# Performance work log

Hardware: AMD Instinct MI355X
Metric: run time of the kernel (lower is better)

Reference implementation:

```python
import jax, jax.numpy as jnp
import numpy as np

EMSIZE = 1024
NHEAD = 16
HEAD = EMSIZE // NHEAD


def setup_inputs() -> dict:
    key = jax.random.key(0)
    ks = jax.random.split(key, 8)
    s = 1.0 / np.sqrt(EMSIZE)
    return {
        "embed": jax.random.normal(ks[0], (2, 2048, EMSIZE), dtype=jnp.float32),
        "q": jax.random.normal(ks[1], (2, 2048, EMSIZE), dtype=jnp.float32),
        "Wk": jax.random.normal(ks[2], (EMSIZE, EMSIZE), dtype=jnp.float32) * s,
        "bk": jnp.zeros((EMSIZE,), dtype=jnp.float32),
        "Wq": jax.random.normal(ks[3], (EMSIZE, EMSIZE), dtype=jnp.float32) * s,
        "bq": jnp.zeros((EMSIZE,), dtype=jnp.float32),
        "Wv": jax.random.normal(ks[4], (EMSIZE, EMSIZE), dtype=jnp.float32) * s,
        "bv": jnp.zeros((EMSIZE,), dtype=jnp.float32),
    }


def _split_heads(x):
    # [b, s, E] -> [b, h, s, d]
    b, s, _ = x.shape
    return x.reshape(b, s, NHEAD, HEAD).transpose(0, 2, 1, 3)


def reference(embed, q, Wk, bk, Wq, bq, Wv, bv):
    # torch Linear: y = x @ W.T + b
    k = _split_heads(embed @ Wk.T + bk)   # [b, h, skv, d]
    qh = _split_heads(q @ Wq.T + bq)      # [b, h, sq, d]
    v = _split_heads(embed @ Wv.T + bv)   # [b, h, skv, d]
    scale = 1.0 / np.sqrt(HEAD).astype(np.float32)
    scores = jnp.einsum("bhqd,bhkd->bhqk", qh, k) * scale
    attn = jax.nn.softmax(scores, axis=-1)  # dropout p=0 -> identity
    ctx = jnp.einsum("bhqk,bhkd->bhqd", attn, v)
    b, h, sq, d = ctx.shape
    return ctx.transpose(0, 2, 1, 3).reshape(b, sq, h * d)
```

## Files before the change

### kernel.cpp

```cpp
#include <hip/hip_runtime.h>
#include <cstdint>
#include <cstddef>


using bf16 = __bf16;
typedef __bf16 bf16x8 __attribute__((ext_vector_type(8)));
typedef float f32x4 __attribute__((ext_vector_type(4)));
typedef float f32x16 __attribute__((ext_vector_type(16)));
using uint32 = unsigned int;

__device__ __forceinline__ void async16(void* lds, const void* g) {
  __builtin_amdgcn_global_load_lds((__attribute__((address_space(1))) void*)g,
                                   (__attribute__((address_space(3))) void*)lds,
                                   16, 0, 0);
}

__device__ __forceinline__ uint32 pack_bf16x2(float lo, float hi_) {
  union { bf16 h[2]; uint32 u; } w;
  w.h[0] = (bf16)lo; w.h[1] = (bf16)hi_;
  return w.u;
}

__global__ void cast_all_kernel(const float* __restrict__ e, const float* __restrict__ q,
                                const float* __restrict__ wk, const float* __restrict__ wq,
                                const float* __restrict__ wv, bf16* __restrict__ dst) {
  int i = blockIdx.x * blockDim.x + threadIdx.x;
  if (i >= 2883584) return;
  const float* src; int off;
  if (i < 1048576)      { src = e;  off = 0; }
  else if (i < 2097152) { src = q;  off = 1048576; }
  else if (i < 2359296) { src = wk; off = 2097152; }
  else if (i < 2621440) { src = wq; off = 2359296; }
  else                  { src = wv; off = 2621440; }
  float4 v = reinterpret_cast<const float4*>(src)[i - off];
  union { bf16 h[4]; unsigned long long u; } o;
  o.h[0] = (bf16)v.x; o.h[1] = (bf16)v.y; o.h[2] = (bf16)v.z; o.h[3] = (bf16)v.w;
  reinterpret_cast<unsigned long long*>(dst)[i] = o.u;
}

__global__ __launch_bounds__(256) void proj_kernel(
    const bf16* __restrict__ emb, const bf16* __restrict__ qin,
    const bf16* __restrict__ wk, const bf16* __restrict__ wq, const bf16* __restrict__ wv,
    const float* __restrict__ bk, const float* __restrict__ bq, const float* __restrict__ bv,
    bf16* __restrict__ Kp, bf16* __restrict__ Qp, bf16* __restrict__ Vt)
{
  __shared__ bf16 As[128 * 64];
  __shared__ bf16 Bs[128 * 64];

  int pid = blockIdx.x;
  int proj = pid >> 8;
  int t = pid & 255;
  int m0 = (t >> 3) * 128;
  int n0 = (t & 7) * 128;

  const bf16* A = (proj == 1) ? qin : emb;
  const bf16* W = (proj == 0) ? wk : (proj == 1) ? wq : wv;
  const float* bias = (proj == 0) ? bk : (proj == 1) ? bq : bv;
  const bool proj2 = (proj == 2);

  int tid = threadIdx.x;
  int lane = tid & 63, wid = tid >> 6;
  int quad = lane >> 4, l16 = lane & 15;
  int moff = (wid & 1) * 64, noff = (wid >> 1) * 64;

  f32x4 zero = {0.f, 0.f, 0.f, 0.f};
  f32x4 acc[4][4];
#pragma unroll
  for (int i = 0; i < 4; i++)
#pragma unroll
    for (int j = 0; j < 4; j++) acc[i][j] = zero;

  for (int kk = 0; kk < 1024; kk += 64) {
    __syncthreads();
#pragma unroll
    for (int i = 0; i < 4; i++) {
      int c = i * 256 + tid;
      int row = c >> 3;
      int ko = ((c ^ row) & 7) << 3;
      async16(&As[(size_t)(i * 256 + wid * 64) * 8], &A[(size_t)(m0 + row) * 1024 + kk + ko]);
      async16(&Bs[(size_t)(i * 256 + wid * 64) * 8], &W[(size_t)(n0 + row) * 1024 + kk + ko]);
    }
    __syncthreads();
#pragma unroll
    for (int ks = 0; ks < 2; ks++) {
      bf16x8 af[4], bfr[4];
#pragma unroll
      for (int i = 0; i < 4; i++) {
        int row = moff + i * 16 + l16;
        af[i] = *reinterpret_cast<const bf16x8*>(&As[row * 64 + ((((ks << 2) | quad) ^ row) & 7) * 8]);
      }
#pragma unroll
      for (int j = 0; j < 4; j++) {
        int row = noff + j * 16 + l16;
        bfr[j] = *reinterpret_cast<const bf16x8*>(&Bs[row * 64 + ((((ks << 2) | quad) ^ row) & 7) * 8]);
      }
      if (proj2) {
#pragma unroll
        for (int i = 0; i < 4; i++)
#pragma unroll
          for (int j = 0; j < 4; j++)
            acc[i][j] = __builtin_amdgcn_mfma_f32_16x16x32_bf16(bfr[j], af[i], acc[i][j], 0, 0, 0);
      } else {
#pragma unroll
        for (int i = 0; i < 4; i++)
#pragma unroll
          for (int j = 0; j < 4; j++)
            acc[i][j] = __builtin_amdgcn_mfma_f32_16x16x32_bf16(af[i], bfr[j], acc[i][j], 0, 0, 0);
      }
    }
  }

  if (proj2) {
#pragma unroll
    for (int i = 0; i < 4; i++) {
      int grow = m0 + moff + i * 16 + l16;
      int bb = grow >> 11;
      int ss = grow & 2047;
#pragma unroll
      for (int j = 0; j < 4; j++) {
#pragma unroll
        for (int r = 0; r < 4; r++) {
          int gcol = n0 + noff + j * 16 + quad * 4 + r;
          int hh = gcol >> 6, dd = gcol & 63;
          int bh = bb * 16 + hh;
          float v = acc[i][j][r] + bias[gcol];
          Vt[((size_t)bh * 64 + dd) * 2048 + ss] = (bf16)v;
        }
      }
    }
  } else {
    float bvv[4];
#pragma unroll
    for (int j = 0; j < 4; j++) bvv[j] = bias[n0 + noff + j * 16 + l16];
    bf16* dst = (proj == 0) ? Kp : Qp;
    const float qs = (proj == 1) ? 0.18033688011112042f : 1.0f;
#pragma unroll
    for (int i = 0; i < 4; i++) {
#pragma unroll
      for (int r = 0; r < 4; r++) {
        int grow = m0 + moff + i * 16 + quad * 4 + r;
        int bb = grow >> 11;
        int ss = grow & 2047;
#pragma unroll
        for (int j = 0; j < 4; j++) {
          int gcol = n0 + noff + j * 16 + l16;
          int hh = gcol >> 6, dd = gcol & 63;
          int bh = bb * 16 + hh;
          float v = (acc[i][j][r] + bvv[j]) * qs;
          dst[((size_t)bh * 2048 + ss) * 64 + dd] = (bf16)v;
        }
      }
    }
  }
}

__global__ __launch_bounds__(512, 4) void attn_kernel(
    const bf16* __restrict__ Qp, const bf16* __restrict__ Kp, const bf16* __restrict__ Vt,
    float* __restrict__ out, float* __restrict__ part1, float* __restrict__ lbuf)
{
  __shared__ bf16 Ks[2][64 * 64];
  __shared__ bf16 Vs[2][64 * 64];

  int bid = blockIdx.x;
  int half = bid & 1;
  int q0 = ((bid >> 1) & 7) << 8;
  int bh = bid >> 4;
  int bb = bh >> 4, hh = bh & 15;
  int g0 = half << 4;

  const bf16* Qg = Qp + (size_t)bh * (2048 * 64);
  const bf16* Kg = Kp + (size_t)bh * (2048 * 64);
  const bf16* Vg = Vt + (size_t)bh * (64 * 2048);

  int tid = threadIdx.x, lane = tid & 63, wid = tid >> 6;
  int l32 = lane & 31;
  int h = lane >> 5;
  int wq0 = q0 + wid * 32;

  auto stage = [&](int kt_, int buf) {
    int c = tid;
    int row = c >> 3;
    int srow = (row & ~12) | ((row & 4) << 1) | ((row & 8) >> 1);
    int ko = ((c ^ row) & 7) << 3;
    async16(&Ks[buf][(size_t)(wid * 64) * 8], &Kg[(size_t)(kt_ * 64 + srow) * 64 + ko]);
    async16(&Vs[buf][(size_t)(wid * 64) * 8], &Vg[(size_t)row * 2048 + kt_ * 64 + ko]);
  };

  bf16x8 qf[4];
#pragma unroll
  for (int s = 0; s < 4; s++)
    qf[s] = *reinterpret_cast<const bf16x8*>(
        &Qg[(size_t)(wq0 + l32) * 64 + s * 16 + h * 8]);

  stage(g0, 0);

  const f32x16 z16 = {0.f, 0.f, 0.f, 0.f, 0.f, 0.f, 0.f, 0.f,
                      0.f, 0.f, 0.f, 0.f, 0.f, 0.f, 0.f, 0.f};
  f32x16 Ov[2];
  Ov[0] = z16; Ov[1] = z16;
  float2 l2;
  l2.x = 0.f; l2.y = 0.f;

  for (int kt = 0; kt < 16; kt++) {
    int cur = kt & 1;
    __syncthreads();
    __builtin_amdgcn_sched_barrier(0);
    if (kt < 15) stage(g0 + kt + 1, cur ^ 1);
    __builtin_amdgcn_sched_barrier(0);

    const bf16* Kc = Ks[cur];
    const bf16* Vc = Vs[cur];

#pragma unroll
    for (int t = 0; t < 2; t++) {
      f32x16 St;
      int row = t * 32 + l32;
      {
        bf16x8 kf = *reinterpret_cast<const bf16x8*>(&Kc[row * 64 + ((h ^ row) & 7) * 8]);
        St = __builtin_amdgcn_mfma_f32_32x32x16_bf16(kf, qf[0], z16, 0, 0, 0);
      }
#pragma unroll
      for (int s = 1; s < 4; s++) {
        int j8 = s * 2 + h;
        bf16x8 kf = *reinterpret_cast<const bf16x8*>(&Kc[row * 64 + ((j8 ^ row) & 7) * 8]);
        St = __builtin_amdgcn_mfma_f32_32x32x16_bf16(kf, qf[s], St, 0, 0, 0);
      }

      uint32 pk[8];
#pragma unroll
      for (int i = 0; i < 8; i++) {
        float pe = __builtin_amdgcn_exp2f(St[2 * i]);
        float po = __builtin_amdgcn_exp2f(St[2 * i + 1]);
        l2.x += pe; l2.y += po;
        pk[i] = pack_bf16x2(pe, po);
      }

#pragma unroll
      for (int g = 0; g < 2; g++) {
        union { uint32 u[4]; bf16x8 v; } pb;
#pragma unroll
        for (int i = 0; i < 4; i++) pb.u[i] = pk[g * 4 + i];
        int j8 = t * 4 + g * 2 + h;
#pragma unroll
        for (int dt = 0; dt < 2; dt++) {
          int rowv = dt * 32 + l32;
          bf16x8 vf = *reinterpret_cast<const bf16x8*>(&Vc[rowv * 64 + ((j8 ^ rowv) & 7) * 8]);
          Ov[dt] = __builtin_amdgcn_mfma_f32_32x32x16_bf16(vf, pb.v, Ov[dt], 0, 0, 0);
        }
      }
    }
  }

  {
    float l_half = l2.x + l2.y;
    float l_tot = l_half + __shfl_xor(l_half, 32);
    int q = wq0 + l32;
    float* dstO = (half == 0 ? out : part1) + ((size_t)bb * 2048 + q) * 1024 + hh * 64;
#pragma unroll
    for (int dt = 0; dt < 2; dt++)
#pragma unroll
      for (int g = 0; g < 4; g++) {
        float4 o;
        o.x = Ov[dt][4 * g + 0];
        o.y = Ov[dt][4 * g + 1];
        o.z = Ov[dt][4 * g + 2];
        o.w = Ov[dt][4 * g + 3];
        *reinterpret_cast<float4*>(&dstO[dt * 32 + g * 8 + 4 * h]) = o;
      }
    if (h == 0) lbuf[half * 65536 + (bh << 11) + q] = l_tot;
  }
}

__global__ __launch_bounds__(256) void combine_kernel(
    float* __restrict__ out, const float* __restrict__ part1,
    const float* __restrict__ lbuf) {
  int i = blockIdx.x * 256 + threadIdx.x;
  int e = i << 2;
  int brow = e >> 10;
  int b = brow >> 11;
  int hcol = (e >> 6) & 15;
  int srow = brow & 2047;
  int lidx = ((b * 16 + hcol) << 11) + srow;
  float inv = 1.0f / (lbuf[lidx] + lbuf[65536 + lidx]);
  float4 a = reinterpret_cast<const float4*>(out)[i];
  float4 p = reinterpret_cast<const float4*>(part1)[i];
  float4 r;
  r.x = (a.x + p.x) * inv;
  r.y = (a.y + p.y) * inv;
  r.z = (a.z + p.z) * inv;
  r.w = (a.w + p.w) * inv;
  reinterpret_cast<float4*>(out)[i] = r;
}

extern "C" void kernel_launch(void* const* d_in, const int* in_sizes, int n_in,
                              void* d_out, int out_size, void* d_ws, size_t ws_size,
                              hipStream_t stream) {
  (void)in_sizes; (void)n_in; (void)out_size; (void)ws_size;
  const float* embed = (const float*)d_in[0];
  const float* qin   = (const float*)d_in[1];
  const float* Wk    = (const float*)d_in[2];
  const float* bk    = (const float*)d_in[3];
  const float* Wq    = (const float*)d_in[4];
  const float* bq    = (const float*)d_in[5];
  const float* Wv    = (const float*)d_in[6];
  const float* bv    = (const float*)d_in[7];
  float* out = (float*)d_out;

  bf16* ws = (bf16*)d_ws;
  bf16* emb_bf = ws;
  bf16* q_bf   = emb_bf + 4194304;
  bf16* wk_bf  = q_bf   + 4194304;
  bf16* wq_bf  = wk_bf  + 1048576;
  bf16* wv_bf  = wq_bf  + 1048576;
  bf16* Kp     = wv_bf  + 1048576;
  bf16* Qp     = Kp     + 4194304;
  bf16* Vt     = Qp     + 4194304;

  float* part1 = (float*)d_ws;
  float* lbuf  = part1 + 4194304;

  cast_all_kernel<<<11264, 256, 0, stream>>>(embed, qin, Wk, Wq, Wv, ws);

  proj_kernel<<<768, 256, 0, stream>>>(emb_bf, q_bf, wk_bf, wq_bf, wv_bf,
                                       bk, bq, bv, Kp, Qp, Vt);
  attn_kernel<<<512, 512, 0, stream>>>(Qp, Kp, Vt, out, part1, lbuf);
  combine_kernel<<<4096, 256, 0, stream>>>(out, part1, lbuf);
}
```

Baseline: 192.5 us.

## Drop split-KV attention and combine kernel; each block covers full key range

Each attention block now processes 128 queries over all 32 key tiles with 256 threads, instead of splitting the key range in two across blocks. The softmax normalisation moves into the attention epilogue, so the separate combine kernel and the fp32 partial-output and row-sum buffers go away. A block-index swizzle spreads consecutive blocks across heads. This removes a launch and roughly two full fp32 output passes through memory, but each block now runs a serial loop twice as long, with fewer waves per block staging the tiles.

```diff
diff --git a/kernel.cpp b/kernel.cpp
--- a/kernel.cpp
+++ b/kernel.cpp
@@ -154,19 +154,18 @@
   }
 }
 
-__global__ __launch_bounds__(512, 4) void attn_kernel(
+__global__ __launch_bounds__(256, 2) void attn_kernel(
     const bf16* __restrict__ Qp, const bf16* __restrict__ Kp, const bf16* __restrict__ Vt,
-    float* __restrict__ out, float* __restrict__ part1, float* __restrict__ lbuf)
+    float* __restrict__ out)
 {
   __shared__ bf16 Ks[2][64 * 64];
   __shared__ bf16 Vs[2][64 * 64];
 
-  int bid = blockIdx.x;
-  int half = bid & 1;
-  int q0 = ((bid >> 1) & 7) << 8;
-  int bh = bid >> 4;
+  int swz = (blockIdx.x & 7) * 64 + (blockIdx.x >> 3);
+  int qblk = swz & 15;
+  int bh = swz >> 4;
+  int q0 = qblk << 7;
   int bb = bh >> 4, hh = bh & 15;
-  int g0 = half << 4;
 
   const bf16* Qg = Qp + (size_t)bh * (2048 * 64);
   const bf16* Kg = Kp + (size_t)bh * (2048 * 64);
@@ -178,12 +177,15 @@
   int wq0 = q0 + wid * 32;
 
   auto stage = [&](int kt_, int buf) {
-    int c = tid;
-    int row = c >> 3;
-    int srow = (row & ~12) | ((row & 4) << 1) | ((row & 8) >> 1);
-    int ko = ((c ^ row) & 7) << 3;
-    async16(&Ks[buf][(size_t)(wid * 64) * 8], &Kg[(size_t)(kt_ * 64 + srow) * 64 + ko]);
-    async16(&Vs[buf][(size_t)(wid * 64) * 8], &Vg[(size_t)row * 2048 + kt_ * 64 + ko]);
+#pragma unroll
+    for (int i = 0; i < 2; i++) {
+      int c = i * 256 + tid;
+      int row = c >> 3;
+      int srow = (row & ~12) | ((row & 4) << 1) | ((row & 8) >> 1);
+      int ko = ((c ^ row) & 7) << 3;
+      async16(&Ks[buf][(size_t)(i * 256 + wid * 64) * 8], &Kg[(size_t)(kt_ * 64 + srow) * 64 + ko]);
+      async16(&Vs[buf][(size_t)(i * 256 + wid * 64) * 8], &Vg[(size_t)row * 2048 + kt_ * 64 + ko]);
+    }
   };
 
   bf16x8 qf[4];
@@ -192,7 +194,7 @@
     qf[s] = *reinterpret_cast<const bf16x8*>(
         &Qg[(size_t)(wq0 + l32) * 64 + s * 16 + h * 8]);
 
-  stage(g0, 0);
+  stage(0, 0);
 
   const f32x16 z16 = {0.f, 0.f, 0.f, 0.f, 0.f, 0.f, 0.f, 0.f,
                       0.f, 0.f, 0.f, 0.f, 0.f, 0.f, 0.f, 0.f};
@@ -201,11 +203,11 @@
   float2 l2;
   l2.x = 0.f; l2.y = 0.f;
 
-  for (int kt = 0; kt < 16; kt++) {
+  for (int kt = 0; kt < 32; kt++) {
     int cur = kt & 1;
     __syncthreads();
     __builtin_amdgcn_sched_barrier(0);
-    if (kt < 15) stage(g0 + kt + 1, cur ^ 1);
+    if (kt < 31) stage(kt + 1, cur ^ 1);
     __builtin_amdgcn_sched_barrier(0);
 
     const bf16* Kc = Ks[cur];
@@ -254,42 +256,21 @@
   {
     float l_half = l2.x + l2.y;
     float l_tot = l_half + __shfl_xor(l_half, 32);
+    float inv = 1.0f / l_tot;
     int q = wq0 + l32;
-    float* dstO = (half == 0 ? out : part1) + ((size_t)bb * 2048 + q) * 1024 + hh * 64;
+    float* dstO = out + ((size_t)bb * 2048 + q) * 1024 + hh * 64;
 #pragma unroll
     for (int dt = 0; dt < 2; dt++)
 #pragma unroll
       for (int g = 0; g < 4; g++) {
         float4 o;
-        o.x = Ov[dt][4 * g + 0];
-        o.y = Ov[dt][4 * g + 1];
-        o.z = Ov[dt][4 * g + 2];
-        o.w = Ov[dt][4 * g + 3];
+        o.x = Ov[dt][4 * g + 0] * inv;
+        o.y = Ov[dt][4 * g + 1] * inv;
+        o.z = Ov[dt][4 * g + 2] * inv;
+        o.w = Ov[dt][4 * g + 3] * inv;
         *reinterpret_cast<float4*>(&dstO[dt * 32 + g * 8 + 4 * h]) = o;
       }
-    if (h == 0) lbuf[half * 65536 + (bh << 11) + q] = l_tot;
   }
-}
-
-__global__ __launch_bounds__(256) void combine_kernel(
-    float* __restrict__ out, const float* __restrict__ part1,
-    const float* __restrict__ lbuf) {
-  int i = blockIdx.x * 256 + threadIdx.x;
-  int e = i << 2;
-  int brow = e >> 10;
-  int b = brow >> 11;
-  int hcol = (e >> 6) & 15;
-  int srow = brow & 2047;
-  int lidx = ((b * 16 + hcol) << 11) + srow;
-  float inv = 1.0f / (lbuf[lidx] + lbuf[65536 + lidx]);
-  float4 a = reinterpret_cast<const float4*>(out)[i];
-  float4 p = reinterpret_cast<const float4*>(part1)[i];
-  float4 r;
-  r.x = (a.x + p.x) * inv;
-  r.y = (a.y + p.y) * inv;
-  r.z = (a.z + p.z) * inv;
-  r.w = (a.w + p.w) * inv;
-  reinterpret_cast<float4*>(out)[i] = r;
 }
 
 extern "C" void kernel_launch(void* const* d_in, const int* in_sizes, int n_in,
@@ -316,13 +297,9 @@
   bf16* Qp     = Kp     + 4194304;
   bf16* Vt     = Qp     + 4194304;
 
-  float* part1 = (float*)d_ws;
-  float* lbuf  = part1 + 4194304;
-
   cast_all_kernel<<<11264, 256, 0, stream>>>(embed, qin, Wk, Wq, Wv, ws);
 
   proj_kernel<<<768, 256, 0, stream>>>(emb_bf, q_bf, wk_bf, wq_bf, wv_bf,
                                        bk, bq, bv, Kp, Qp, Vt);
-  attn_kernel<<<512, 512, 0, stream>>>(Qp, Kp, Vt, out, part1, lbuf);
-  combine_kernel<<<4096, 256, 0, stream>>>(out, part1, lbuf);
-}
+  attn_kernel<<<512, 256, 0, stream>>>(Qp, Kp, Vt, out);
+}
```

Result: faster. 187.2 us (-2.8%).
